# Kernel tuning notes

Hardware: AMD Instinct MI355X
Metric: run time of the kernel (lower is better)

The kernel has to match this reference:

```python
import jax, jax.numpy as jnp
import numpy as np

N_NODES = 100000
N_EDGES = 1600000
N_GRAPHS = 128
BEHAVIOR_DIM = 32
LLM_DIM = 768
LLM_PROJ = 32
HIDDEN = 64
NUM_CLASSES = 2
INPUT_DIM = 64 + 16 + LLM_PROJ + BEHAVIOR_DIM  # 144


def gcn_conv(h, edge_index, edge_weight, W, b, n):
    """PyG GCNConv: linear -> gcn_norm with self-loops -> scatter-add at target."""
    h = h @ W  # [N, out]
    row, col = edge_index[0], edge_index[1]
    loop = jnp.arange(n)
    row_f = jnp.concatenate([row, loop])
    col_f = jnp.concatenate([col, loop])
    ew_f = jnp.concatenate([edge_weight, jnp.ones((n,), h.dtype)])
    deg = jax.ops.segment_sum(ew_f, col_f, num_segments=n)
    dinv = jnp.where(deg > 0, jax.lax.rsqrt(deg), 0.0)
    norm = dinv[row_f] * ew_f * dinv[col_f]  # [E+N]
    out = jax.ops.segment_sum(norm[:, None] * h[row_f], col_f, num_segments=n)
    return out + b


def global_mean_pool(x, batch, num_graphs):
    s = jax.ops.segment_sum(x, batch, num_segments=num_graphs)
    cnt = jax.ops.segment_sum(jnp.ones((x.shape[0],), x.dtype), batch, num_segments=num_graphs)
    return s / jnp.maximum(cnt, 1.0)[:, None]


def setup_inputs() -> dict:
    key = jax.random.key(0)
    ks = jax.random.split(key, 16)
    inp = {
        "x_names": jax.random.randint(ks[0], (N_NODES,), 0, 20000),
        "x_types": jax.random.randint(ks[1], (N_NODES,), 0, 100),
        "x_behaviors": jax.random.normal(ks[2], (N_NODES, BEHAVIOR_DIM), jnp.float32),
        "edge_index": jax.random.randint(ks[3], (2, N_EDGES), 0, N_NODES),
        "edge_weight": jax.random.uniform(ks[4], (N_EDGES,), jnp.float32),
        "batch": jnp.sort(jax.random.randint(ks[5], (N_NODES,), 0, N_GRAPHS)),
        "llm_features": jax.random.normal(ks[6], (N_NODES, LLM_DIM), jnp.float32),
        # parameters
        "name_emb": jax.random.normal(ks[7], (20000, 64), jnp.float32),
        "type_emb": jax.random.normal(ks[8], (100, 16), jnp.float32),
        "llm_proj_w": jax.random.normal(ks[9], (LLM_DIM, LLM_PROJ), jnp.float32) * 0.02,
        "llm_proj_b": jnp.zeros((LLM_PROJ,), jnp.float32),
        "conv1_w": jax.random.normal(ks[10], (INPUT_DIM, HIDDEN), jnp.float32) * 0.08,
        "conv1_b": jnp.zeros((HIDDEN,), jnp.float32),
        "conv2_w": jax.random.normal(ks[11], (HIDDEN, HIDDEN), jnp.float32) * 0.12,
        "conv2_b": jnp.zeros((HIDDEN,), jnp.float32),
        "cls_w": jax.random.normal(ks[12], (HIDDEN, NUM_CLASSES), jnp.float32) * 0.12,
        "cls_b": jnp.zeros((NUM_CLASSES,), jnp.float32),
    }
    return inp


def reference(x_names, x_types, x_behaviors, edge_index, edge_weight, batch,
              llm_features, name_emb, type_emb, llm_proj_w, llm_proj_b,
              conv1_w, conv1_b, conv2_w, conv2_b, cls_w, cls_b):
    n = x_names.shape[0]
    name_feat = name_emb[x_names]          # [N, 64]
    type_feat = type_emb[x_types]          # [N, 16]
    llm_feat = llm_features @ llm_proj_w + llm_proj_b  # [N, 32]
    x = jnp.concatenate([name_feat, type_feat, llm_feat, x_behaviors], axis=1)
    # dropout is identity in eval mode
    x = jax.nn.relu(gcn_conv(x, edge_index, edge_weight, conv1_w, conv1_b, n))
    x = jax.nn.relu(gcn_conv(x, edge_index, edge_weight, conv2_w, conv2_b, n))
    x = global_mean_pool(x, batch, N_GRAPHS)  # [G, HIDDEN]
    return x @ cls_w + cls_b                   # [G, 2]
```

## Files before the change

### kernel.cpp

```cpp
#include <hip/hip_runtime.h>
#include <cstdint>
#include <cstddef>

typedef __attribute__((ext_vector_type(8))) short bf16x8;
typedef __attribute__((ext_vector_type(4))) float f32x4;


__device__ __forceinline__ unsigned bf_rne(float x) {
  unsigned u = __float_as_uint(x);
  return (u + 0x7FFFu + ((u >> 16) & 1u)) >> 16;
}

__device__ __forceinline__ void split1(float x, short& hi, short& lo) {
  unsigned hb = bf_rne(x);
  hi = (short)hb;
  float fh = __uint_as_float(hb << 16);
  lo = (short)bf_rne(x - fh);
}

__device__ __forceinline__ void split8(const float4& p, const float4& q, bf16x8& h, bf16x8& l) {
  short hh, ll;
  split1(p.x, hh, ll); h[0] = hh; l[0] = ll;
  split1(p.y, hh, ll); h[1] = hh; l[1] = ll;
  split1(p.z, hh, ll); h[2] = hh; l[2] = ll;
  split1(p.w, hh, ll); h[3] = hh; l[3] = ll;
  split1(q.x, hh, ll); h[4] = hh; l[4] = ll;
  split1(q.y, hh, ll); h[5] = hh; l[5] = ll;
  split1(q.z, hh, ll); h[6] = hh; l[6] = ll;
  split1(q.w, hh, ll); h[7] = hh; l[7] = ll;
}


__global__ void prep1_kernel(const float* __restrict__ pw, const float* __restrict__ pb,
                             const float* __restrict__ w1,
                             short* __restrict__ Bh, short* __restrict__ Bl,
                             float* __restrict__ biasf) {
  int idx = blockIdx.x * 256 + threadIdx.x;
  if (idx < 896 * 64) {
    int gk = idx >> 6, col = idx & 63;
    float val;
    if (gk < 768) {
      float acc = 0.0f;
      #pragma unroll 8
      for (int m = 0; m < 32; ++m) acc = fmaf(pw[gk * 32 + m], w1[(80 + m) * 64 + col], acc);
      val = acc;
    } else if (gk < 832) val = w1[(gk - 768) * 64 + col];
    else if (gk < 848)   val = w1[(64 + gk - 832) * 64 + col];
    else if (gk < 864)   val = w1[(112 + gk - 848) * 64 + col];
    else if (gk < 880)   val = w1[(128 + gk - 864) * 64 + col];
    else                 val = 0.0f;
    int chunk = gk >> 5, k = gk & 31;
    int g, j;
    if (k < 16) { g = k >> 2; j = k & 3; } else { int k2 = k - 16; g = k2 >> 2; j = 4 + (k2 & 3); }
    size_t o = ((size_t)(chunk * 4 + g) * 64 + col) * 8 + j;
    short hh, ll; split1(val, hh, ll);
    Bh[o] = hh; Bl[o] = ll;
  } else if (idx < 896 * 64 + 64) {
    int col = idx - 896 * 64;
    float acc = 0.0f;
    for (int m = 0; m < 32; ++m) acc = fmaf(pb[m], w1[(80 + m) * 64 + col], acc);
    biasf[col] = acc;
  }
}

__global__ void prep2_kernel(const float* __restrict__ w2,
                             short* __restrict__ B2h, short* __restrict__ B2l) {
  int idx = blockIdx.x * 256 + threadIdx.x;
  if (idx >= 64 * 64) return;
  int gk = idx >> 6, col = idx & 63;
  float val = w2[gk * 64 + col];
  int chunk = gk >> 5, k = gk & 31;
  int g, j;
  if (k < 16) { g = k >> 2; j = k & 3; } else { int k2 = k - 16; g = k2 >> 2; j = 4 + (k2 & 3); }
  size_t o = ((size_t)(chunk * 4 + g) * 64 + col) * 8 + j;
  short hh, ll; split1(val, hh, ll);
  B2h[o] = hh; B2l[o] = ll;
}


__global__ void zero_kernel(int* __restrict__ cnt, int n) {
  int i = blockIdx.x * 256 + threadIdx.x;
  if (i < n) cnt[i] = 0;
}

__global__ void cnt_kernel(const int* __restrict__ ei, int* __restrict__ cnt, int E) {
  int e = blockIdx.x * 256 + threadIdx.x;
  if (e < E) atomicAdd(&cnt[ei[E + e]], 1);
}

__global__ __launch_bounds__(256) void scan_blk(const int* __restrict__ cnt,
                                                int* __restrict__ colp,
                                                int* __restrict__ bsum, int n) {
  __shared__ int ws[4];
  int t = threadIdx.x, lane = t & 63, w = t >> 6;
  int i = blockIdx.x * 256 + t;
  int v = (i < n) ? cnt[i] : 0;
  int x = v;
  #pragma unroll
  for (int off = 1; off < 64; off <<= 1) { int y = __shfl_up(x, off); if (lane >= off) x += y; }
  if (lane == 63) ws[w] = x;
  __syncthreads();
  if (t == 0) {
    int s = 0;
    #pragma unroll
    for (int k = 0; k < 4; ++k) { int tmp = ws[k]; ws[k] = s; s += tmp; }
    bsum[blockIdx.x] = s;
  }
  __syncthreads();
  if (i < n) colp[i] = ws[w] + x - v;
}

__global__ __launch_bounds__(512) void scan_top(int* __restrict__ bsum,
                                                int* __restrict__ colp, int nb, int n) {
  __shared__ int ws[8];
  int t = threadIdx.x, lane = t & 63, w = t >> 6;
  int v = (t < nb) ? bsum[t] : 0;
  int x = v;
  #pragma unroll
  for (int off = 1; off < 64; off <<= 1) { int y = __shfl_up(x, off); if (lane >= off) x += y; }
  if (lane == 63) ws[w] = x;
  __syncthreads();
  if (t == 0) {
    int s = 0;
    #pragma unroll
    for (int k = 0; k < 8; ++k) { int tmp = ws[k]; ws[k] = s; s += tmp; }
  }
  __syncthreads();
  int excl = ws[w] + x - v;
  if (t < nb) bsum[t] = excl;
  if (t == nb - 1) colp[n] = excl + v;
}

__global__ void scan_add(int* __restrict__ colp, int* __restrict__ fillp,
                         const int* __restrict__ bsum, int n) {
  int i = blockIdx.x * 256 + threadIdx.x;
  if (i < n) {
    int c = colp[i] + bsum[blockIdx.x];
    colp[i] = c;
    fillp[i] = c;
  }
}

__global__ void fill_kernel(const int* __restrict__ ei, const float* __restrict__ ew,
                            int* __restrict__ fillp, int2* __restrict__ csr, int E) {
  int e = blockIdx.x * 256 + threadIdx.x;
  if (e >= E) return;
  int row = ei[e], col = ei[E + e];
  int pos = atomicAdd(&fillp[col], 1);
  csr[pos] = make_int2(row, __float_as_int(ew[e]));
}

__global__ void degsum_kernel(const int* __restrict__ colp, const int2* __restrict__ csr,
                              float* __restrict__ dinv, int n) {
  int j = blockIdx.x * 256 + threadIdx.x;
  if (j >= n) return;
  int e0 = colp[j], e1 = colp[j + 1];
  float s = 1.0f;
  for (int e = e0; e < e1; ++e) s += __int_as_float(csr[e].y);
  dinv[j] = rsqrtf(s);
}

__global__ void wfix_kernel(int2* __restrict__ csr, const float* __restrict__ dinv, int E) {
  int i = blockIdx.x * 256 + threadIdx.x;
  if (i >= E) return;
  int2 m = csr[i];
  csr[i] = make_int2(m.x, __float_as_int(__int_as_float(m.y) * dinv[m.x]));
}


__device__ __forceinline__ void loadA1(int c, int arow, bool inb, int nm, int tp, int g,
                                       const float* __restrict__ llm,
                                       const float* __restrict__ nemb,
                                       const float* __restrict__ temb,
                                       const float* __restrict__ beh,
                                       float4& lo, float4& hi) {
  const float4 z = make_float4(0.f, 0.f, 0.f, 0.f);
  if (c < 24) {
    const float* p = llm + (size_t)arow * 768 + c * 32 + g * 4;
    lo = inb ? *(const float4*)p : z;
    hi = inb ? *(const float4*)(p + 16) : z;
  } else if (c < 26) {
    const float* p = nemb + (size_t)nm * 64 + (c - 24) * 32 + g * 4;
    lo = *(const float4*)p;
    hi = *(const float4*)(p + 16);
  } else if (c == 26) {
    lo = *(const float4*)(temb + (size_t)tp * 16 + g * 4);
    hi = inb ? *(const float4*)(beh + (size_t)arow * 32 + g * 4) : z;
  } else {
    lo = inb ? *(const float4*)(beh + (size_t)arow * 32 + 16 + g * 4) : z;
    hi = z;
  }
}

__global__ __launch_bounds__(256, 4) void gemm1_kernel(
    const float* __restrict__ llm, const short* __restrict__ Bh, const short* __restrict__ Bl,
    const int* __restrict__ names, const int* __restrict__ types,
    const float* __restrict__ beh, const float* __restrict__ nemb,
    const float* __restrict__ temb, const float* __restrict__ biasf,
    float* __restrict__ out, int n)
{
  int w = blockIdx.x * 4 + (threadIdx.x >> 6);
  int nw = (n + 31) >> 5;
  if (w >= nw) return;
  int lane = threadIdx.x & 63;
  int g = lane >> 4, r16 = lane & 15;
  int base = w * 32;

  int arow0 = base + r16, arow1 = base + 16 + r16;
  bool inb0 = arow0 < n, inb1 = arow1 < n;
  int nm0 = inb0 ? names[arow0] : 0;
  int nm1 = inb1 ? names[arow1] : 0;
  int tp0 = inb0 ? types[arow0] : 0;
  int tp1 = inb1 ? types[arow1] : 0;

  f32x4 acc[2][4];
  #pragma unroll
  for (int i = 0; i < 2; ++i)
    #pragma unroll
    for (int j = 0; j < 4; ++j) { acc[i][j][0] = 0.f; acc[i][j][1] = 0.f; acc[i][j][2] = 0.f; acc[i][j][3] = 0.f; }

  float4 aLo0, aHi0, aLo1, aHi1, nLo0, nHi0, nLo1, nHi1;
  loadA1(0, arow0, inb0, nm0, tp0, g, llm, nemb, temb, beh, aLo0, aHi0);
  loadA1(0, arow1, inb1, nm1, tp1, g, llm, nemb, temb, beh, aLo1, aHi1);

  #pragma unroll 1
  for (int c = 0; c < 28; ++c) {
    bf16x8 bh[4], bl[4];
    #pragma unroll
    for (int ct = 0; ct < 4; ++ct) {
      size_t o = ((size_t)(c * 4 + g) * 64 + ct * 16 + r16) * 8;
      bh[ct] = *(const bf16x8*)(Bh + o);
      bl[ct] = *(const bf16x8*)(Bl + o);
    }
    if (c < 27) {
      loadA1(c + 1, arow0, inb0, nm0, tp0, g, llm, nemb, temb, beh, nLo0, nHi0);
      loadA1(c + 1, arow1, inb1, nm1, tp1, g, llm, nemb, temb, beh, nLo1, nHi1);
    }
    bf16x8 ah, al;
    split8(aLo0, aHi0, ah, al);
    #pragma unroll
    for (int ct = 0; ct < 4; ++ct) {
      acc[0][ct] = __builtin_amdgcn_mfma_f32_16x16x32_bf16(ah, bh[ct], acc[0][ct], 0, 0, 0);
      acc[0][ct] = __builtin_amdgcn_mfma_f32_16x16x32_bf16(ah, bl[ct], acc[0][ct], 0, 0, 0);
      acc[0][ct] = __builtin_amdgcn_mfma_f32_16x16x32_bf16(al, bh[ct], acc[0][ct], 0, 0, 0);
    }
    split8(aLo1, aHi1, ah, al);
    #pragma unroll
    for (int ct = 0; ct < 4; ++ct) {
      acc[1][ct] = __builtin_amdgcn_mfma_f32_16x16x32_bf16(ah, bh[ct], acc[1][ct], 0, 0, 0);
      acc[1][ct] = __builtin_amdgcn_mfma_f32_16x16x32_bf16(ah, bl[ct], acc[1][ct], 0, 0, 0);
      acc[1][ct] = __builtin_amdgcn_mfma_f32_16x16x32_bf16(al, bh[ct], acc[1][ct], 0, 0, 0);
    }
    aLo0 = nLo0; aHi0 = nHi0; aLo1 = nLo1; aHi1 = nHi1;
  }

  #pragma unroll
  for (int ct = 0; ct < 4; ++ct) {
    int col = ct * 16 + r16;
    float bf = biasf[col];
    #pragma unroll
    for (int rr = 0; rr < 4; ++rr) {
      int node0 = base + g * 4 + rr;
      if (node0 < n) out[(size_t)node0 * 64 + col] = acc[0][ct][rr] + bf;
      int node1 = base + 16 + g * 4 + rr;
      if (node1 < n) out[(size_t)node1 * 64 + col] = acc[1][ct][rr] + bf;
    }
  }
}


__global__ __launch_bounds__(256, 4) void gemm2_kernel(
    const float* __restrict__ h, const short* __restrict__ B2h, const short* __restrict__ B2l,
    float* __restrict__ out, int n)
{
  int w = blockIdx.x * 4 + (threadIdx.x >> 6);
  int nw = (n + 31) >> 5;
  if (w >= nw) return;
  int lane = threadIdx.x & 63;
  int g = lane >> 4, r16 = lane & 15;
  int base = w * 32;
  int arow0 = base + r16, arow1 = base + 16 + r16;
  bool inb0 = arow0 < n, inb1 = arow1 < n;
  const float4 z = make_float4(0.f, 0.f, 0.f, 0.f);

  f32x4 acc[2][4];
  #pragma unroll
  for (int i = 0; i < 2; ++i)
    #pragma unroll
    for (int j = 0; j < 4; ++j) { acc[i][j][0] = 0.f; acc[i][j][1] = 0.f; acc[i][j][2] = 0.f; acc[i][j][3] = 0.f; }

  #pragma unroll
  for (int c = 0; c < 2; ++c) {
    bf16x8 bh[4], bl[4];
    #pragma unroll
    for (int ct = 0; ct < 4; ++ct) {
      size_t o = ((size_t)(c * 4 + g) * 64 + ct * 16 + r16) * 8;
      bh[ct] = *(const bf16x8*)(B2h + o);
      bl[ct] = *(const bf16x8*)(B2l + o);
    }
    const float* p0 = h + (size_t)arow0 * 64 + c * 32 + g * 4;
    const float* p1 = h + (size_t)arow1 * 64 + c * 32 + g * 4;
    float4 lo0 = inb0 ? *(const float4*)p0 : z;
    float4 hi0 = inb0 ? *(const float4*)(p0 + 16) : z;
    float4 lo1 = inb1 ? *(const float4*)p1 : z;
    float4 hi1 = inb1 ? *(const float4*)(p1 + 16) : z;
    bf16x8 ah, al;
    split8(lo0, hi0, ah, al);
    #pragma unroll
    for (int ct = 0; ct < 4; ++ct) {
      acc[0][ct] = __builtin_amdgcn_mfma_f32_16x16x32_bf16(ah, bh[ct], acc[0][ct], 0, 0, 0);
      acc[0][ct] = __builtin_amdgcn_mfma_f32_16x16x32_bf16(ah, bl[ct], acc[0][ct], 0, 0, 0);
      acc[0][ct] = __builtin_amdgcn_mfma_f32_16x16x32_bf16(al, bh[ct], acc[0][ct], 0, 0, 0);
    }
    split8(lo1, hi1, ah, al);
    #pragma unroll
    for (int ct = 0; ct < 4; ++ct) {
      acc[1][ct] = __builtin_amdgcn_mfma_f32_16x16x32_bf16(ah, bh[ct], acc[1][ct], 0, 0, 0);
      acc[1][ct] = __builtin_amdgcn_mfma_f32_16x16x32_bf16(ah, bl[ct], acc[1][ct], 0, 0, 0);
      acc[1][ct] = __builtin_amdgcn_mfma_f32_16x16x32_bf16(al, bh[ct], acc[1][ct], 0, 0, 0);
    }
  }

  #pragma unroll
  for (int ct = 0; ct < 4; ++ct) {
    int col = ct * 16 + r16;
    #pragma unroll
    for (int rr = 0; rr < 4; ++rr) {
      int node0 = base + g * 4 + rr;
      if (node0 < n) out[(size_t)node0 * 64 + col] = acc[0][ct][rr];
      int node1 = base + 16 + g * 4 + rr;
      if (node1 < n) out[(size_t)node1 * 64 + col] = acc[1][ct][rr];
    }
  }
}


__global__ __launch_bounds__(256) void agg_kernel(
    const float* __restrict__ h, const int* __restrict__ colp,
    const int2* __restrict__ csr, const float* __restrict__ dinv,
    const float* __restrict__ bias, float* __restrict__ out, int n)
{
  int wid = threadIdx.x >> 6, lane = threadIdx.x & 63;
  int j = blockIdx.x * 4 + wid;
  if (j >= n) return;
  float dj = dinv[j];
  float hj = h[(size_t)j * 64 + lane];
  int e0 = colp[j], e1 = colp[j + 1];
  float s = 0.0f;
  int e = e0;
  for (; e + 4 <= e1; e += 4) {
    int2 m0 = csr[e], m1 = csr[e + 1], m2 = csr[e + 2], m3 = csr[e + 3];
    float f0 = h[(size_t)m0.x * 64 + lane];
    float f1 = h[(size_t)m1.x * 64 + lane];
    float f2 = h[(size_t)m2.x * 64 + lane];
    float f3 = h[(size_t)m3.x * 64 + lane];
    s = fmaf(__int_as_float(m0.y), f0, s);
    s = fmaf(__int_as_float(m1.y), f1, s);
    s = fmaf(__int_as_float(m2.y), f2, s);
    s = fmaf(__int_as_float(m3.y), f3, s);
  }
  for (; e < e1; ++e) {
    int2 m = csr[e];
    s = fmaf(__int_as_float(m.y), h[(size_t)m.x * 64 + lane], s);
  }
  float acc = bias[lane] + dj * fmaf(dj, hj, s);
  out[(size_t)j * 64 + lane] = fmaxf(acc, 0.0f);
}


__global__ __launch_bounds__(256) void pool_kernel(const float* __restrict__ x,
                                                   const int* __restrict__ batch,
                                                   float* __restrict__ pooled, int n) {
  __shared__ float red[4][64];
  __shared__ int range_s[2];
  int gph = blockIdx.x;
  int tid = threadIdx.x, wid = tid >> 6, lane = tid & 63;
  if (tid < 2) {
    int target = gph + tid;
    int lo = 0, hi = n;
    while (lo < hi) { int m = (lo + hi) >> 1; if (batch[m] < target) lo = m + 1; else hi = m; }
    range_s[tid] = lo;
  }
  __syncthreads();
  int lo = range_s[0], hi = range_s[1];
  float acc = 0.0f;
  for (int i = lo + wid; i < hi; i += 4) acc += x[(size_t)i * 64 + lane];
  red[wid][lane] = acc;
  __syncthreads();
  if (tid < 64) {
    float sum = red[0][lane] + red[1][lane] + red[2][lane] + red[3][lane];
    float cntf = (float)(hi - lo);
    pooled[gph * 64 + lane] = sum / fmaxf(cntf, 1.0f);
  }
}

__global__ void cls_kernel(const float* __restrict__ pooled, const float* __restrict__ cw,
                           const float* __restrict__ cb, float* __restrict__ out) {
  int t = threadIdx.x;
  int gph = t >> 1, c = t & 1;
  float acc = cb[c];
  #pragma unroll 8
  for (int k = 0; k < 64; ++k) acc = fmaf(pooled[gph * 64 + k], cw[k * 2 + c], acc);
  out[gph * 2 + c] = acc;
}


extern "C" void kernel_launch(void* const* d_in, const int* in_sizes, int n_in,
                              void* d_out, int out_size, void* d_ws, size_t ws_size,
                              hipStream_t stream) {
  const int*   x_names  = (const int*)  d_in[0];
  const int*   x_types  = (const int*)  d_in[1];
  const float* behav    = (const float*)d_in[2];
  const int*   ei       = (const int*)  d_in[3];
  const float* ew       = (const float*)d_in[4];
  const int*   batch    = (const int*)  d_in[5];
  const float* llm      = (const float*)d_in[6];
  const float* name_emb = (const float*)d_in[7];
  const float* type_emb = (const float*)d_in[8];
  const float* pw       = (const float*)d_in[9];
  const float* pb       = (const float*)d_in[10];
  const float* w1       = (const float*)d_in[11];
  const float* b1       = (const float*)d_in[12];
  const float* w2       = (const float*)d_in[13];
  const float* b2       = (const float*)d_in[14];
  const float* cw       = (const float*)d_in[15];
  const float* cb       = (const float*)d_in[16];

  const int N = in_sizes[0];
  const int E = in_sizes[4];
  const int nb = (N + 255) / 256;
  const int eb = (E + 255) / 256;
  const int nwaves = (N + 31) / 32;
  const int gblocks = (nwaves + 3) / 4;

  char* p = (char*)d_ws;
  auto alloc = [&](size_t bytes) -> void* {
    void* r = (void*)p; p += (bytes + 255) & ~(size_t)255; return r;
  };
  float* dinv   = (float*)alloc((size_t)N * 4);
  int*   cnt    = (int*)  alloc((size_t)N * 4);
  int*   colp   = (int*)  alloc((size_t)(N + 1) * 4);
  int*   fillp  = (int*)  alloc((size_t)N * 4);
  int2*  csr    = (int2*) alloc((size_t)E * 8);
  int*   bsum   = (int*)  alloc((size_t)(nb + 1) * 4);
  short* Bh     = (short*)alloc((size_t)896 * 64 * 2);
  short* Bl     = (short*)alloc((size_t)896 * 64 * 2);
  short* B2h    = (short*)alloc((size_t)64 * 64 * 2);
  short* B2l    = (short*)alloc((size_t)64 * 64 * 2);
  float* biasf  = (float*)alloc((size_t)64 * 4);
  float* bufX   = (float*)alloc((size_t)N * 64 * 4);
  float* bufY   = (float*)alloc((size_t)N * 64 * 4);
  float* pooled = (float*)alloc((size_t)128 * 64 * 4);
  (void)ws_size; (void)n_in; (void)out_size;

  prep1_kernel<<<(896 * 64 + 64 + 255) / 256, 256, 0, stream>>>(pw, pb, w1, Bh, Bl, biasf);
  prep2_kernel<<<16, 256, 0, stream>>>(w2, B2h, B2l);
  zero_kernel<<<nb, 256, 0, stream>>>(cnt, N);
  cnt_kernel<<<eb, 256, 0, stream>>>(ei, cnt, E);
  scan_blk<<<nb, 256, 0, stream>>>(cnt, colp, bsum, N);
  scan_top<<<1, 512, 0, stream>>>(bsum, colp, nb, N);
  scan_add<<<nb, 256, 0, stream>>>(colp, fillp, bsum, N);
  fill_kernel<<<eb, 256, 0, stream>>>(ei, ew, fillp, csr, E);
  degsum_kernel<<<nb, 256, 0, stream>>>(colp, csr, dinv, N);
  wfix_kernel<<<eb, 256, 0, stream>>>(csr, dinv, E);

  gemm1_kernel<<<gblocks, 256, 0, stream>>>(llm, Bh, Bl, x_names, x_types, behav,
                                            name_emb, type_emb, biasf, bufX, N);
  agg_kernel<<<(N + 3) / 4, 256, 0, stream>>>(bufX, colp, csr, dinv, b1, bufY, N);
  gemm2_kernel<<<gblocks, 256, 0, stream>>>(bufY, B2h, B2l, bufX, N);
  agg_kernel<<<(N + 3) / 4, 256, 0, stream>>>(bufX, colp, csr, dinv, b2, bufY, N);
  pool_kernel<<<128, 256, 0, stream>>>(bufY, batch, pooled, N);
  cls_kernel<<<1, 256, 0, stream>>>(pooled, cw, cb, (float*)d_out);
}
```

Before: 587.5 us.

## Restructure gemm1 main loop with two-deep A prefetch and XCD-aware block swizzle

The gemm1 loop is split into a steady LLM-feature phase with two stages of A-tile prefetch kept in registers, followed by separate epilogue blocks for the name, type and behavior features. This removes the per-iteration branching in the loader. Blocks are remapped so consecutive tiles land on the same XCD, which is meant to improve L2 locality. Out-of-range rows are clamped instead of predicated. Occupancy hint drops from 4 to 3 blocks per CU to make room for the extra prefetch registers. The zero kernel is replaced with hipMemsetAsync.

```diff
diff --git a/kernel.cpp b/kernel.cpp
--- a/kernel.cpp
+++ b/kernel.cpp
@@ -78,11 +78,6 @@
 }
 
 
-__global__ void zero_kernel(int* __restrict__ cnt, int n) {
-  int i = blockIdx.x * 256 + threadIdx.x;
-  if (i < n) cnt[i] = 0;
-}
-
 __global__ void cnt_kernel(const int* __restrict__ ei, int* __restrict__ cnt, int E) {
   int e = blockIdx.x * 256 + threadIdx.x;
   if (e < E) atomicAdd(&cnt[ei[E + e]], 1);
@@ -168,50 +163,61 @@
 }
 
 
-__device__ __forceinline__ void loadA1(int c, int arow, bool inb, int nm, int tp, int g,
-                                       const float* __restrict__ llm,
-                                       const float* __restrict__ nemb,
-                                       const float* __restrict__ temb,
-                                       const float* __restrict__ beh,
-                                       float4& lo, float4& hi) {
-  const float4 z = make_float4(0.f, 0.f, 0.f, 0.f);
-  if (c < 24) {
-    const float* p = llm + (size_t)arow * 768 + c * 32 + g * 4;
-    lo = inb ? *(const float4*)p : z;
-    hi = inb ? *(const float4*)(p + 16) : z;
-  } else if (c < 26) {
-    const float* p = nemb + (size_t)nm * 64 + (c - 24) * 32 + g * 4;
-    lo = *(const float4*)p;
-    hi = *(const float4*)(p + 16);
-  } else if (c == 26) {
-    lo = *(const float4*)(temb + (size_t)tp * 16 + g * 4);
-    hi = inb ? *(const float4*)(beh + (size_t)arow * 32 + g * 4) : z;
-  } else {
-    lo = inb ? *(const float4*)(beh + (size_t)arow * 32 + 16 + g * 4) : z;
-    hi = z;
-  }
-}
-
-__global__ __launch_bounds__(256, 4) void gemm1_kernel(
+__device__ __forceinline__ void mfma24(f32x4 (&acc)[2][4],
+                                       const bf16x8& ah0, const bf16x8& al0,
+                                       const bf16x8& ah1, const bf16x8& al1,
+                                       const bf16x8 (&bh)[4], const bf16x8 (&bl)[4]) {
+  #pragma unroll
+  for (int ct = 0; ct < 4; ++ct) {
+    acc[0][ct] = __builtin_amdgcn_mfma_f32_16x16x32_bf16(ah0, bh[ct], acc[0][ct], 0, 0, 0);
+    acc[0][ct] = __builtin_amdgcn_mfma_f32_16x16x32_bf16(ah0, bl[ct], acc[0][ct], 0, 0, 0);
+    acc[0][ct] = __builtin_amdgcn_mfma_f32_16x16x32_bf16(al0, bh[ct], acc[0][ct], 0, 0, 0);
+  }
+  #pragma unroll
+  for (int ct = 0; ct < 4; ++ct) {
+    acc[1][ct] = __builtin_amdgcn_mfma_f32_16x16x32_bf16(ah1, bh[ct], acc[1][ct], 0, 0, 0);
+    acc[1][ct] = __builtin_amdgcn_mfma_f32_16x16x32_bf16(ah1, bl[ct], acc[1][ct], 0, 0, 0);
+    acc[1][ct] = __builtin_amdgcn_mfma_f32_16x16x32_bf16(al1, bh[ct], acc[1][ct], 0, 0, 0);
+  }
+}
+
+__device__ __forceinline__ void loadB(const short* __restrict__ Bh, const short* __restrict__ Bl,
+                                      int c, int g, int r16, bf16x8 (&bh)[4], bf16x8 (&bl)[4]) {
+  #pragma unroll
+  for (int ct = 0; ct < 4; ++ct) {
+    size_t o = ((size_t)(c * 4 + g) * 64 + ct * 16 + r16) * 8;
+    bh[ct] = *(const bf16x8*)(Bh + o);
+    bl[ct] = *(const bf16x8*)(Bl + o);
+  }
+}
+
+__global__ __launch_bounds__(256, 3) void gemm1_kernel(
     const float* __restrict__ llm, const short* __restrict__ Bh, const short* __restrict__ Bl,
     const int* __restrict__ names, const int* __restrict__ types,
     const float* __restrict__ beh, const float* __restrict__ nemb,
     const float* __restrict__ temb, const float* __restrict__ biasf,
     float* __restrict__ out, int n)
 {
-  int w = blockIdx.x * 4 + (threadIdx.x >> 6);
+  int nwg = gridDim.x;
+  int b = blockIdx.x;
+  int q = nwg >> 3, r = nwg & 7;
+  int xcd = b & 7, idx = b >> 3;
+  int swz = (xcd < r ? xcd * (q + 1) : r * (q + 1) + (xcd - r) * q) + idx;
+
+  int w = swz * 4 + (threadIdx.x >> 6);
   int nw = (n + 31) >> 5;
   if (w >= nw) return;
   int lane = threadIdx.x & 63;
   int g = lane >> 4, r16 = lane & 15;
   int base = w * 32;
 
-  int arow0 = base + r16, arow1 = base + 16 + r16;
-  bool inb0 = arow0 < n, inb1 = arow1 < n;
-  int nm0 = inb0 ? names[arow0] : 0;
-  int nm1 = inb1 ? names[arow1] : 0;
-  int tp0 = inb0 ? types[arow0] : 0;
-  int tp1 = inb1 ? types[arow1] : 0;
+  int arow0 = base + r16;      if (arow0 > n - 1) arow0 = n - 1;
+  int arow1 = base + 16 + r16; if (arow1 > n - 1) arow1 = n - 1;
+  int nm0 = names[arow0], nm1 = names[arow1];
+  int tp0 = types[arow0], tp1 = types[arow1];
+
+  const float* pA0 = llm + (size_t)arow0 * 768 + g * 4;
+  const float* pA1 = llm + (size_t)arow1 * 768 + g * 4;
 
   f32x4 acc[2][4];
   #pragma unroll
@@ -219,39 +225,73 @@
     #pragma unroll
     for (int j = 0; j < 4; ++j) { acc[i][j][0] = 0.f; acc[i][j][1] = 0.f; acc[i][j][2] = 0.f; acc[i][j][3] = 0.f; }
 
-  float4 aLo0, aHi0, aLo1, aHi1, nLo0, nHi0, nLo1, nHi1;
-  loadA1(0, arow0, inb0, nm0, tp0, g, llm, nemb, temb, beh, aLo0, aHi0);
-  loadA1(0, arow1, inb1, nm1, tp1, g, llm, nemb, temb, beh, aLo1, aHi1);
+  float4 X0l = *(const float4*)(pA0 +  0), X0h = *(const float4*)(pA0 + 16);
+  float4 X1l = *(const float4*)(pA1 +  0), X1h = *(const float4*)(pA1 + 16);
+  float4 Y0l = *(const float4*)(pA0 + 32), Y0h = *(const float4*)(pA0 + 48);
+  float4 Y1l = *(const float4*)(pA1 + 32), Y1h = *(const float4*)(pA1 + 48);
+
+  bf16x8 bh[4], bl[4], ah0, al0, ah1, al1;
 
   #pragma unroll 1
-  for (int c = 0; c < 28; ++c) {
-    bf16x8 bh[4], bl[4];
-    #pragma unroll
-    for (int ct = 0; ct < 4; ++ct) {
-      size_t o = ((size_t)(c * 4 + g) * 64 + ct * 16 + r16) * 8;
-      bh[ct] = *(const bf16x8*)(Bh + o);
-      bl[ct] = *(const bf16x8*)(Bl + o);
-    }
-    if (c < 27) {
-      loadA1(c + 1, arow0, inb0, nm0, tp0, g, llm, nemb, temb, beh, nLo0, nHi0);
-      loadA1(c + 1, arow1, inb1, nm1, tp1, g, llm, nemb, temb, beh, nLo1, nHi1);
-    }
-    bf16x8 ah, al;
-    split8(aLo0, aHi0, ah, al);
-    #pragma unroll
-    for (int ct = 0; ct < 4; ++ct) {
-      acc[0][ct] = __builtin_amdgcn_mfma_f32_16x16x32_bf16(ah, bh[ct], acc[0][ct], 0, 0, 0);
-      acc[0][ct] = __builtin_amdgcn_mfma_f32_16x16x32_bf16(ah, bl[ct], acc[0][ct], 0, 0, 0);
-      acc[0][ct] = __builtin_amdgcn_mfma_f32_16x16x32_bf16(al, bh[ct], acc[0][ct], 0, 0, 0);
-    }
-    split8(aLo1, aHi1, ah, al);
-    #pragma unroll
-    for (int ct = 0; ct < 4; ++ct) {
-      acc[1][ct] = __builtin_amdgcn_mfma_f32_16x16x32_bf16(ah, bh[ct], acc[1][ct], 0, 0, 0);
-      acc[1][ct] = __builtin_amdgcn_mfma_f32_16x16x32_bf16(ah, bl[ct], acc[1][ct], 0, 0, 0);
-      acc[1][ct] = __builtin_amdgcn_mfma_f32_16x16x32_bf16(al, bh[ct], acc[1][ct], 0, 0, 0);
-    }
-    aLo0 = nLo0; aHi0 = nHi0; aLo1 = nLo1; aHi1 = nHi1;
+  for (int cc = 0; cc < 11; ++cc) {
+    const int c = cc * 2;
+    loadB(Bh, Bl, c, g, r16, bh, bl);
+    split8(X0l, X0h, ah0, al0);
+    split8(X1l, X1h, ah1, al1);
+    X0l = *(const float4*)(pA0 + (c + 2) * 32);
+    X0h = *(const float4*)(pA0 + (c + 2) * 32 + 16);
+    X1l = *(const float4*)(pA1 + (c + 2) * 32);
+    X1h = *(const float4*)(pA1 + (c + 2) * 32 + 16);
+    mfma24(acc, ah0, al0, ah1, al1, bh, bl);
+    loadB(Bh, Bl, c + 1, g, r16, bh, bl);
+    split8(Y0l, Y0h, ah0, al0);
+    split8(Y1l, Y1h, ah1, al1);
+    Y0l = *(const float4*)(pA0 + (c + 3) * 32);
+    Y0h = *(const float4*)(pA0 + (c + 3) * 32 + 16);
+    Y1l = *(const float4*)(pA1 + (c + 3) * 32);
+    Y1h = *(const float4*)(pA1 + (c + 3) * 32 + 16);
+    mfma24(acc, ah0, al0, ah1, al1, bh, bl);
+  }
+
+  loadB(Bh, Bl, 22, g, r16, bh, bl);
+  split8(X0l, X0h, ah0, al0);
+  split8(X1l, X1h, ah1, al1);
+  mfma24(acc, ah0, al0, ah1, al1, bh, bl);
+
+  loadB(Bh, Bl, 23, g, r16, bh, bl);
+  split8(Y0l, Y0h, ah0, al0);
+  split8(Y1l, Y1h, ah1, al1);
+  mfma24(acc, ah0, al0, ah1, al1, bh, bl);
+
+  const float* pN0 = nemb + (size_t)nm0 * 64 + g * 4;
+  const float* pN1 = nemb + (size_t)nm1 * 64 + g * 4;
+  #pragma unroll
+  for (int t = 0; t < 2; ++t) {
+    float4 l0 = *(const float4*)(pN0 + t * 32), h0 = *(const float4*)(pN0 + t * 32 + 16);
+    float4 l1 = *(const float4*)(pN1 + t * 32), h1 = *(const float4*)(pN1 + t * 32 + 16);
+    loadB(Bh, Bl, 24 + t, g, r16, bh, bl);
+    split8(l0, h0, ah0, al0);
+    split8(l1, h1, ah1, al1);
+    mfma24(acc, ah0, al0, ah1, al1, bh, bl);
+  }
+  {
+    float4 l0 = *(const float4*)(temb + (size_t)tp0 * 16 + g * 4);
+    float4 h0 = *(const float4*)(beh + (size_t)arow0 * 32 + g * 4);
+    float4 l1 = *(const float4*)(temb + (size_t)tp1 * 16 + g * 4);
+    float4 h1 = *(const float4*)(beh + (size_t)arow1 * 32 + g * 4);
+    loadB(Bh, Bl, 26, g, r16, bh, bl);
+    split8(l0, h0, ah0, al0);
+    split8(l1, h1, ah1, al1);
+    mfma24(acc, ah0, al0, ah1, al1, bh, bl);
+  }
+  {
+    const float4 z = make_float4(0.f, 0.f, 0.f, 0.f);
+    float4 l0 = *(const float4*)(beh + (size_t)arow0 * 32 + 16 + g * 4);
+    float4 l1 = *(const float4*)(beh + (size_t)arow1 * 32 + 16 + g * 4);
+    loadB(Bh, Bl, 27, g, r16, bh, bl);
+    split8(l0, z, ah0, al0);
+    split8(l1, z, ah1, al1);
+    mfma24(acc, ah0, al0, ah1, al1, bh, bl);
   }
 
   #pragma unroll
@@ -279,9 +319,8 @@
   int lane = threadIdx.x & 63;
   int g = lane >> 4, r16 = lane & 15;
   int base = w * 32;
-  int arow0 = base + r16, arow1 = base + 16 + r16;
-  bool inb0 = arow0 < n, inb1 = arow1 < n;
-  const float4 z = make_float4(0.f, 0.f, 0.f, 0.f);
+  int arow0 = base + r16;      if (arow0 > n - 1) arow0 = n - 1;
+  int arow1 = base + 16 + r16; if (arow1 > n - 1) arow1 = n - 1;
 
   f32x4 acc[2][4];
   #pragma unroll
@@ -292,33 +331,15 @@
   #pragma unroll
   for (int c = 0; c < 2; ++c) {
     bf16x8 bh[4], bl[4];
-    #pragma unroll
-    for (int ct = 0; ct < 4; ++ct) {
-      size_t o = ((size_t)(c * 4 + g) * 64 + ct * 16 + r16) * 8;
-      bh[ct] = *(const bf16x8*)(B2h + o);
-      bl[ct] = *(const bf16x8*)(B2l + o);
-    }
+    loadB(B2h, B2l, c, g, r16, bh, bl);
     const float* p0 = h + (size_t)arow0 * 64 + c * 32 + g * 4;
     const float* p1 = h + (size_t)arow1 * 64 + c * 32 + g * 4;
-    float4 lo0 = inb0 ? *(const float4*)p0 : z;
-    float4 hi0 = inb0 ? *(const float4*)(p0 + 16) : z;
-    float4 lo1 = inb1 ? *(const float4*)p1 : z;
-    float4 hi1 = inb1 ? *(const float4*)(p1 + 16) : z;
-    bf16x8 ah, al;
-    split8(lo0, hi0, ah, al);
-    #pragma unroll
-    for (int ct = 0; ct < 4; ++ct) {
-      acc[0][ct] = __builtin_amdgcn_mfma_f32_16x16x32_bf16(ah, bh[ct], acc[0][ct], 0, 0, 0);
-      acc[0][ct] = __builtin_amdgcn_mfma_f32_16x16x32_bf16(ah, bl[ct], acc[0][ct], 0, 0, 0);
-      acc[0][ct] = __builtin_amdgcn_mfma_f32_16x16x32_bf16(al, bh[ct], acc[0][ct], 0, 0, 0);
-    }
-    split8(lo1, hi1, ah, al);
-    #pragma unroll
-    for (int ct = 0; ct < 4; ++ct) {
-      acc[1][ct] = __builtin_amdgcn_mfma_f32_16x16x32_bf16(ah, bh[ct], acc[1][ct], 0, 0, 0);
-      acc[1][ct] = __builtin_amdgcn_mfma_f32_16x16x32_bf16(ah, bl[ct], acc[1][ct], 0, 0, 0);
-      acc[1][ct] = __builtin_amdgcn_mfma_f32_16x16x32_bf16(al, bh[ct], acc[1][ct], 0, 0, 0);
-    }
+    float4 lo0 = *(const float4*)p0, hi0 = *(const float4*)(p0 + 16);
+    float4 lo1 = *(const float4*)p1, hi1 = *(const float4*)(p1 + 16);
+    bf16x8 ah0, al0, ah1, al1;
+    split8(lo0, hi0, ah0, al0);
+    split8(lo1, hi1, ah1, al1);
+    mfma24(acc, ah0, al0, ah1, al1, bh, bl);
   }
 
   #pragma unroll
@@ -455,7 +476,7 @@
 
   prep1_kernel<<<(896 * 64 + 64 + 255) / 256, 256, 0, stream>>>(pw, pb, w1, Bh, Bl, biasf);
   prep2_kernel<<<16, 256, 0, stream>>>(w2, B2h, B2l);
-  zero_kernel<<<nb, 256, 0, stream>>>(cnt, N);
+  hipMemsetAsync(cnt, 0, (size_t)N * 4, stream);
   cnt_kernel<<<eb, 256, 0, stream>>>(ei, cnt, E);
   scan_blk<<<nb, 256, 0, stream>>>(cnt, colp, bsum, N);
   scan_top<<<1, 512, 0, stream>>>(bsum, colp, nb, N);
```

New measurement: 548.2 us. 1.07x faster.
